# Kernel tuning notes

Hardware: AMD Instinct MI355X
Metric: run time of the kernel (lower is better)

Reference implementation:

```python
import jax, jax.numpy as jnp
import numpy as np

LOG2PI = float(np.log(2.0 * np.pi))

# Each Gaussian g is exp(-0.5*(a_g.x + b_g.y + c_g)^2)/sqrt(2*pi), with x the H current
# hidden variables and y the H next hidden variables. The original module applies a
# precompiled sequence of Givens-rotation 'gaussian products' (sequence_phase_1/2) that
# (phase 1) zero the x-coefficients of all but one pivot Gaussian per variable and
# integrate the pivots out, then (phase 2) rotate the leftover Gaussians so only H of
# them depend on y; leftover pure-bias Gaussians contribute norm_log_gaussian(bias).
# A sequence of Givens rotations is an orthogonal transform of the rows [a|b|c], so the
# whole procedure equals (up to per-row signs, which leave every Gaussian invariant):
#   QR on A -> integrate H pivots: LC1 = -sum_j log|R1_jj|
#   project B,c onto A's orthogonal complement, QR on PB -> kept rows (R2, Q2^T Pc)
#   residual bias energy -> LC2 = -0.5*((K-H)*log(2pi) + ||(P - Q2 Q2^T) c||^2)


def setup_inputs() -> dict:
    B, P, H, K, D = 2048, 4, 16, 48, 4
    key = jax.random.key(0)
    ks = jax.random.split(key, 8)
    f32 = jnp.float32
    return {
        "input_i": jax.random.normal(ks[0], (B, P, D), dtype=f32),
        "Prev_coefs": jax.random.normal(ks[1], (H, B, P, H), dtype=f32),
        "Prev_biases": jax.random.normal(ks[2], (H, B, P), dtype=f32),
        "LP": jnp.zeros((B, P), dtype=f32),
        "Log_factors": jax.random.normal(ks[3], (B, P), dtype=f32),
        "obs_var_coefs": jax.random.normal(ks[4], (K, B, P, D), dtype=f32),
        "hidden_var_coefs": jax.random.normal(ks[5], (K, B, P, H), dtype=f32),
        "next_hidden_var_coefs": jax.random.normal(ks[6], (K, B, P, H), dtype=f32),
        "rec_biases": jax.random.normal(ks[7], (K, B, P), dtype=f32),
    }


def reference(input_i, Prev_coefs, Prev_biases, LP, Log_factors,
              obs_var_coefs, hidden_var_coefs, next_hidden_var_coefs, rec_biases):
    H = Prev_coefs.shape[0]
    K = rec_biases.shape[0]
    # observation contribution to the recurrent Gaussians' biases: [K,B,P]
    cur_b = rec_biases + jnp.sum(obs_var_coefs * input_i[None], axis=-1)
    # stack all G = H + K Gaussians: coefs on current hidden vars (A), next hidden
    # vars (Bm) and biases (c). Previous-step Gaussians have zero next-var coefs.
    A = jnp.concatenate([Prev_coefs, hidden_var_coefs], axis=0)            # [G,B,P,H]
    Bm = jnp.concatenate([jnp.zeros_like(Prev_coefs), next_hidden_var_coefs], 0)
    c = jnp.concatenate([Prev_biases, cur_b], axis=0)                      # [G,B,P]
    A = jnp.moveaxis(A, 0, 2)   # [B,P,G,H]
    Bm = jnp.moveaxis(Bm, 0, 2)  # [B,P,G,H]
    c = jnp.moveaxis(c, 0, 2)   # [B,P,G]

    # phase 1: orthogonal elimination of the current-hidden-variable coefficients,
    # then integrate the H pivot Gaussians out.
    Q1, R1 = jnp.linalg.qr(A)                                              # Q1 [B,P,G,H]
    diag1 = jnp.abs(jnp.diagonal(R1, axis1=-2, axis2=-1))
    LC = -jnp.sum(jnp.log(diag1), axis=-1)                                 # [B,P]
    # project next-var coefs and biases onto the orthogonal complement of span(A)
    PB = Bm - Q1 @ (jnp.swapaxes(Q1, -1, -2) @ Bm)                         # [B,P,G,H]
    Pc = c - jnp.einsum('bpgh,bph->bpg', Q1, jnp.einsum('bpgh,bpg->bph', Q1, c))

    # phase 2: reduce the remaining K Gaussians to H kept ones.
    Q2, R2 = jnp.linalg.qr(PB)                                             # R2 [B,P,H,H]
    nb = jnp.einsum('bpgh,bpg->bph', Q2, Pc)                               # kept biases
    resid = jnp.maximum(jnp.sum(Pc * Pc, -1) - jnp.sum(nb * nb, -1), 0.0)
    # leftover (K - H) pure-bias Gaussians: sum of norm_log_gaussian(bias)
    LC = LC - 0.5 * ((K - H) * LOG2PI + resid)

    LP_new = LP + LC + Log_factors
    Next_coefs = jnp.moveaxis(R2, 2, 0)    # [H,B,P,H]
    Next_biases = jnp.moveaxis(nb, -1, 0)  # [H,B,P]
    return (Next_coefs, Next_biases, LP_new)
```

## Files before the change

kernel.cpp:

```cpp
#include <hip/hip_runtime.h>

#define LOG2PI 1.8378770664093453

__device__ __forceinline__ float rl32(float v, int l) {
  return __int_as_float(__builtin_amdgcn_readlane(__float_as_int(v), l));
}

__global__ __launch_bounds__(128, 6) void cint_kernel(
    const float* __restrict__ input_i,
    const float* __restrict__ Prev_coefs,
    const float* __restrict__ Prev_biases,
    const float* __restrict__ LPin,
    const float* __restrict__ Log_factors,
    const float* __restrict__ obs_var,
    const float* __restrict__ hid_var,
    const float* __restrict__ nxt_var,
    const float* __restrict__ rec_biases,
    float* __restrict__ out,
    int NBP)
{
  __shared__ float X[64*36];
  __shared__ float S[16*36];
  __shared__ float M2[2];

  const int tid  = threadIdx.x;
  const int w    = tid >> 6;
  const int lane = tid & 63;
  const int bid  = blockIdx.x;
  const int inst = (bid & 7) * (NBP >> 3) + (bid >> 3);

  float* PB = X;
  float* G  = S;

  const size_t NB_OFFv = (size_t)NBP * 256;
  const size_t LP_OFFv = NB_OFFv + (size_t)NBP * 16;

  const float lp_lf = LPin[inst] + Log_factors[inst];

  {
    const int g = lane;
    const size_t rowidx = (g < 16) ? ((size_t)g * NBP + inst)
                                   : ((size_t)(g - 16) * NBP + inst);
    if (w == 0) {
      const float* aptr = (g < 16) ? (Prev_coefs + rowidx * 16)
                                   : (hid_var    + rowidx * 16);
      *(float4*)&X[g*36 +  0] = *(const float4*)(aptr + 0);
      *(float4*)&X[g*36 +  4] = *(const float4*)(aptr + 4);
      *(float4*)&X[g*36 +  8] = *(const float4*)(aptr + 8);
      *(float4*)&X[g*36 + 12] = *(const float4*)(aptr + 12);
    } else {
      float4 z4 = make_float4(0.f, 0.f, 0.f, 0.f);
      float4 b0 = z4, b1 = z4, b2 = z4, b3 = z4;
      float cv;
      if (g < 16) {
        cv = Prev_biases[rowidx];
      } else {
        const float* bptr = nxt_var + rowidx * 16;
        b0 = *(const float4*)(bptr + 0);
        b1 = *(const float4*)(bptr + 4);
        b2 = *(const float4*)(bptr + 8);
        b3 = *(const float4*)(bptr + 12);
        float4 ob = *(const float4*)(obs_var + rowidx * 4);
        float4 iv = *(const float4*)(input_i + (size_t)inst * 4);
        cv = rec_biases[rowidx] + ob.x*iv.x + ob.y*iv.y + ob.z*iv.z + ob.w*iv.w;
      }
      *(float4*)&X[g*36 + 16] = b0;
      *(float4*)&X[g*36 + 20] = b1;
      *(float4*)&X[g*36 + 24] = b2;
      *(float4*)&X[g*36 + 28] = b3;
      X[g*36 + 32] = cv;
    }
  }
  __syncthreads();

  {
    const int i  = tid & 15;
    const int st = tid >> 4;
    float ac0=0, ac1=0, ac2=0, ac3=0, ac4=0;
    #pragma unroll 8
    for (int g = 0; g < 64; ++g) {
      const float* xr = &X[g*36];
      float  xi = xr[i];
      float4 cv = *(const float4*)(xr + 4*st);
      ac0 = fmaf(xi, cv.x, ac0);
      ac1 = fmaf(xi, cv.y, ac1);
      ac2 = fmaf(xi, cv.z, ac2);
      ac3 = fmaf(xi, cv.w, ac3);
      if (st == 0) ac4 = fmaf(xi, xr[32], ac4);
    }
    float* srow = &S[i*36 + 4*st];
    srow[0]=ac0; srow[1]=ac1; srow[2]=ac2; srow[3]=ac3;
    if (st == 0) S[i*36 + 32] = ac4;
  }
  __syncthreads();

  if (w == 0) {
    float Lr[16];
    {
      const int ir = lane & 15;
      double prodd = 1.0;
      #pragma unroll
      for (int j = 0; j < 16; ++j) {
        float s = S[ir*36 + j];
        #pragma unroll
        for (int m = 0; m < j; ++m) s = fmaf(-Lr[m], rl32(Lr[m], j), s);
        float sj = rl32(s, j);
        sj = fmaxf(sj, 1e-30f);
        float Ljj = sqrtf(sj);
        float iv  = 1.0f / Ljj;
        prodd *= (double)sj;
        Lr[j] = (ir == j) ? Ljj : s * iv;
        if (lane == j) S[j*36 + 33] = iv;
      }
      if (lane == 0) M2[1] = (float)(-0.5 * log(prodd));
    }
    {
      const int rc = (lane < 17) ? lane : 16;
      float x[16];
      #pragma unroll
      for (int j = 0; j < 16; ++j) {
        float t = S[j*36 + 16 + rc];
        #pragma unroll
        for (int m = 0; m < j; ++m) t = fmaf(-rl32(Lr[m], j), x[m], t);
        x[j] = t * S[j*36 + 33];
      }
      #pragma unroll
      for (int j = 15; j >= 0; --j) {
        float t = x[j];
        #pragma unroll
        for (int m = j + 1; m < 16; ++m) t = fmaf(-rl32(Lr[j], m), x[m], t);
        x[j] = t * S[j*36 + 33];
      }
      if (lane < 17) {
        #pragma unroll
        for (int m = 0; m < 16; ++m) S[m*36 + 16 + lane] = x[m];
      }
    }
  }
  __syncthreads();

  {
    const int g = lane;
    const float* xr = &X[g*36];
    float4 a0 = *(const float4*)(xr + 0);
    float4 a1 = *(const float4*)(xr + 4);
    float4 a2 = *(const float4*)(xr + 8);
    float4 a3 = *(const float4*)(xr + 12);
    float ad[16] = { a0.x,a0.y,a0.z,a0.w, a1.x,a1.y,a1.z,a1.w,
                     a2.x,a2.y,a2.z,a2.w, a3.x,a3.y,a3.z,a3.w };
    float4 e0, e1; float pc = 0.0f;
    if (w == 0) {
      e0 = *(const float4*)(xr + 16);
      e1 = *(const float4*)(xr + 20);
    } else {
      e0 = *(const float4*)(xr + 24);
      e1 = *(const float4*)(xr + 28);
      pc = xr[32];
    }
    float pb[8] = { e0.x,e0.y,e0.z,e0.w, e1.x,e1.y,e1.z,e1.w };
    __syncthreads();
    const int coff = 16 + 8*w;
    #pragma unroll
    for (int m = 0; m < 16; ++m) {
      float am = ad[m];
      float4 w0v = *(const float4*)(&S[m*36 + coff]);
      float4 w1v = *(const float4*)(&S[m*36 + coff + 4]);
      pb[0] = fmaf(-am, w0v.x, pb[0]); pb[1] = fmaf(-am, w0v.y, pb[1]);
      pb[2] = fmaf(-am, w0v.z, pb[2]); pb[3] = fmaf(-am, w0v.w, pb[3]);
      pb[4] = fmaf(-am, w1v.x, pb[4]); pb[5] = fmaf(-am, w1v.y, pb[5]);
      pb[6] = fmaf(-am, w1v.z, pb[6]); pb[7] = fmaf(-am, w1v.w, pb[7]);
      if (w == 1) pc = fmaf(-am, S[m*36 + 32], pc);
    }
    if (w == 1) {
      float q = pc * pc;
      #pragma unroll
      for (int msk = 1; msk < 64; msk <<= 1) q += __shfl_xor(q, msk, 64);
      if (lane == 0) M2[0] = q;
    }
    float4 o0 = { pb[0], pb[1], pb[2], pb[3] };
    float4 o1 = { pb[4], pb[5], pb[6], pb[7] };
    *(float4*)&PB[g*20 + 8*w + 0] = o0;
    *(float4*)&PB[g*20 + 8*w + 4] = o1;
    if (w == 1) PB[g*20 + 16] = pc;
  }
  __syncthreads();

  {
    const int k1 = tid & 15;
    const int q  = tid >> 4;
    float ac0=0, ac1=0, ac4=0;
    #pragma unroll 8
    for (int g = 0; g < 64; ++g) {
      const float* pr = &PB[g*20];
      float  xr = pr[k1];
      float2 cv = *(const float2*)(pr + 2*q);
      ac0 = fmaf(xr, cv.x, ac0);
      ac1 = fmaf(xr, cv.y, ac1);
      if (q == 0) ac4 = fmaf(xr, pr[16], ac4);
    }
    G[k1*18 + 2*q]     = ac0;
    G[k1*18 + 2*q + 1] = ac1;
    if (q == 0) G[k1*18 + 16] = ac4;
  }
  __syncthreads();

  if (w == 0) {
    const int k  = lane;
    const int kc = (k < 17) ? k : 16;
    float Tr[16];
    float Gh[16];
    #pragma unroll
    for (int r = 0; r < 16; ++r) Tr[r] = PB[r*20 + kc];
    #pragma unroll
    for (int j = 0; j < 16; ++j) Gh[j] = G[j*18 + kc];
    float nbacc = 0.0f;
    #pragma unroll
    for (int j = 0; j < 16; ++j) {
      float alf  = rl32(Tr[j], j);
      float nrm2 = rl32(Gh[j], j);
      float nrm  = sqrtf(fmaxf(nrm2, 1e-30f));
      float aa   = fabsf(alf);
      float tau  = 1.0f + aa / nrm;
      float inv  = copysignf(1.0f / (aa + nrm), alf);
      float beta = -copysignf(nrm, alf);
      float Tj   = Tr[j];
      float wv   = Tj + (Gh[j] - alf * Tj) * inv;
      float Rv   = Tj - tau * wv;
      if (k < 16) {
        float ov = (k < j) ? 0.0f : ((k == j) ? beta : Rv);
        out[((size_t)j * NBP + inst) * 16 + k] = ov;
      } else if (k == 16) {
        out[NB_OFFv + (size_t)j * NBP + inst] = Rv;
        nbacc = fmaf(Rv, Rv, nbacc);
      }
      float twi = tau * wv * inv;
      #pragma unroll
      for (int r = j + 1; r < 16; ++r) {
        float vr = rl32(Tr[r], j);
        Tr[r] = fmaf(-twi, vr, Tr[r]);
      }
      #pragma unroll
      for (int l = j + 1; l < 16; ++l) {
        float Rl = rl32(Rv, l);
        Gh[l] = fmaf(-Rl, Rv, Gh[l]);
      }
    }
    if (k == 16) {
      double resid = fmax((double)M2[0] - (double)nbacc, 0.0);
      double LC = (double)M2[1] - 0.5 * (32.0 * LOG2PI + resid);
      out[LP_OFFv + (size_t)inst] = lp_lf + (float)LC;
    }
  }
}

extern "C" void kernel_launch(void* const* d_in, const int* in_sizes, int n_in,
                              void* d_out, int out_size, void* d_ws, size_t ws_size,
                              hipStream_t stream) {
  (void)n_in; (void)out_size; (void)d_ws; (void)ws_size;
  const int NBP = in_sizes[3];
  cint_kernel<<<NBP, 128, 0, stream>>>(
      (const float*)d_in[0], (const float*)d_in[1], (const float*)d_in[2],
      (const float*)d_in[3], (const float*)d_in[4], (const float*)d_in[5],
      (const float*)d_in[6], (const float*)d_in[7], (const float*)d_in[8],
      (float*)d_out, NBP);
}
```

Baseline: 186.4 us.

## Compute full Gram matrix once and derive projected Gram via Schur complement

Instead of forming the projected matrix PB explicitly over all 64 rows and then computing its Gram matrix, the kernel computes the full 33x33 symmetric Gram of [A|B|c] once (lower triangle split across threads) and obtains the projected Gram and the top rows of PB through triangular solves with the Cholesky factor (Schur complement). This drops one 64-row pass and the back-substitution, shares a single LDS buffer, and raises the occupancy hint to 7. In exchange it relies on the Gram/Schur formulation being numerically adequate, and it adds slot-mapping overhead and extra LDS transposes.

```diff
diff --git a/kernel.cpp b/kernel.cpp
--- a/kernel.cpp
+++ b/kernel.cpp
@@ -6,7 +6,30 @@
   return __int_as_float(__builtin_amdgcn_readlane(__float_as_int(v), l));
 }
 
-__global__ __launch_bounds__(128, 6) void cint_kernel(
+#define OFF_M33   0
+#define OFF_STAB  1188
+#define OFF_T     1188
+#define OFF_Y     1508
+#define OFF_Z     1828
+#define OFF_G     2148
+#define OFF_CTOP  2454
+#define OFF_ATOPT 2470
+#define OFF_M2    2790
+#define LDSZ      2792
+
+__device__ __forceinline__ void slot_to_rq(int s, int& r, int& q) {
+  if      (s < 4)   { r = s;               q = 0;    }
+  else if (s < 12)  { int i=s-4;   r=4 +i/2; q=i-(i/2)*2; }
+  else if (s < 24)  { int i=s-12;  r=8 +i/3; q=i-(i/3)*3; }
+  else if (s < 40)  { int i=s-24;  r=12+(i>>2); q=i&3; }
+  else if (s < 60)  { int i=s-40;  r=16+i/5; q=i-(i/5)*5; }
+  else if (s < 84)  { int i=s-60;  r=20+i/6; q=i-(i/6)*6; }
+  else if (s < 112) { int i=s-84;  r=24+i/7; q=i-(i/7)*7; }
+  else if (s < 144) { int i=s-112; r=28+(i>>3); q=i&7; }
+  else              { r = 32; q = s-144; }
+}
+
+__global__ __launch_bounds__(128, 7) void cint_kernel(
     const float* __restrict__ input_i,
     const float* __restrict__ Prev_coefs,
     const float* __restrict__ Prev_biases,
@@ -19,18 +42,13 @@
     float* __restrict__ out,
     int NBP)
 {
-  __shared__ float X[64*36];
-  __shared__ float S[16*36];
-  __shared__ float M2[2];
+  __shared__ float lds[LDSZ];
 
   const int tid  = threadIdx.x;
   const int w    = tid >> 6;
   const int lane = tid & 63;
   const int bid  = blockIdx.x;
   const int inst = (bid & 7) * (NBP >> 3) + (bid >> 3);
-
-  float* PB = X;
-  float* G  = S;
 
   const size_t NB_OFFv = (size_t)NBP * 256;
   const size_t LP_OFFv = NB_OFFv + (size_t)NBP * 16;
@@ -44,16 +62,31 @@
     if (w == 0) {
       const float* aptr = (g < 16) ? (Prev_coefs + rowidx * 16)
                                    : (hid_var    + rowidx * 16);
-      *(float4*)&X[g*36 +  0] = *(const float4*)(aptr + 0);
-      *(float4*)&X[g*36 +  4] = *(const float4*)(aptr + 4);
-      *(float4*)&X[g*36 +  8] = *(const float4*)(aptr + 8);
-      *(float4*)&X[g*36 + 12] = *(const float4*)(aptr + 12);
+      float4 a0 = *(const float4*)(aptr + 0);
+      float4 a1 = *(const float4*)(aptr + 4);
+      float4 a2 = *(const float4*)(aptr + 8);
+      float4 a3 = *(const float4*)(aptr + 12);
+      *(float4*)&lds[g*36 +  0] = a0;
+      *(float4*)&lds[g*36 +  4] = a1;
+      *(float4*)&lds[g*36 +  8] = a2;
+      *(float4*)&lds[g*36 + 12] = a3;
+      if (g < 16) {
+        lds[OFF_ATOPT +  0*20+g]=a0.x; lds[OFF_ATOPT +  1*20+g]=a0.y;
+        lds[OFF_ATOPT +  2*20+g]=a0.z; lds[OFF_ATOPT +  3*20+g]=a0.w;
+        lds[OFF_ATOPT +  4*20+g]=a1.x; lds[OFF_ATOPT +  5*20+g]=a1.y;
+        lds[OFF_ATOPT +  6*20+g]=a1.z; lds[OFF_ATOPT +  7*20+g]=a1.w;
+        lds[OFF_ATOPT +  8*20+g]=a2.x; lds[OFF_ATOPT +  9*20+g]=a2.y;
+        lds[OFF_ATOPT + 10*20+g]=a2.z; lds[OFF_ATOPT + 11*20+g]=a2.w;
+        lds[OFF_ATOPT + 12*20+g]=a3.x; lds[OFF_ATOPT + 13*20+g]=a3.y;
+        lds[OFF_ATOPT + 14*20+g]=a3.z; lds[OFF_ATOPT + 15*20+g]=a3.w;
+      }
     } else {
       float4 z4 = make_float4(0.f, 0.f, 0.f, 0.f);
       float4 b0 = z4, b1 = z4, b2 = z4, b3 = z4;
       float cv;
       if (g < 16) {
         cv = Prev_biases[rowidx];
+        lds[OFF_CTOP + g] = cv;
       } else {
         const float* bptr = nxt_var + rowidx * 16;
         b0 = *(const float4*)(bptr + 0);
@@ -64,33 +97,65 @@
         float4 iv = *(const float4*)(input_i + (size_t)inst * 4);
         cv = rec_biases[rowidx] + ob.x*iv.x + ob.y*iv.y + ob.z*iv.z + ob.w*iv.w;
       }
-      *(float4*)&X[g*36 + 16] = b0;
-      *(float4*)&X[g*36 + 20] = b1;
-      *(float4*)&X[g*36 + 24] = b2;
-      *(float4*)&X[g*36 + 28] = b3;
-      X[g*36 + 32] = cv;
-    }
-  }
-  __syncthreads();
-
-  {
-    const int i  = tid & 15;
-    const int st = tid >> 4;
-    float ac0=0, ac1=0, ac2=0, ac3=0, ac4=0;
+      *(float4*)&lds[g*36 + 16] = b0;
+      *(float4*)&lds[g*36 + 20] = b1;
+      *(float4*)&lds[g*36 + 24] = b2;
+      *(float4*)&lds[g*36 + 28] = b3;
+      lds[g*36 + 32] = cv;
+      lds[g*36 + 33] = 0.f; lds[g*36 + 34] = 0.f; lds[g*36 + 35] = 0.f;
+    }
+  }
+  __syncthreads();
+
+  int r0, q0; slot_to_rq(tid, r0, q0);
+  float a00=0,a01=0,a02=0,a03=0;
+  {
     #pragma unroll 8
     for (int g = 0; g < 64; ++g) {
-      const float* xr = &X[g*36];
-      float  xi = xr[i];
-      float4 cv = *(const float4*)(xr + 4*st);
-      ac0 = fmaf(xi, cv.x, ac0);
-      ac1 = fmaf(xi, cv.y, ac1);
-      ac2 = fmaf(xi, cv.z, ac2);
-      ac3 = fmaf(xi, cv.w, ac3);
-      if (st == 0) ac4 = fmaf(xi, xr[32], ac4);
-    }
-    float* srow = &S[i*36 + 4*st];
-    srow[0]=ac0; srow[1]=ac1; srow[2]=ac2; srow[3]=ac3;
-    if (st == 0) S[i*36 + 32] = ac4;
+      const float* xr = &lds[g*36];
+      float  xi = xr[r0];
+      float4 cv = *(const float4*)(xr + 4*q0);
+      a00=fmaf(xi,cv.x,a00); a01=fmaf(xi,cv.y,a01);
+      a02=fmaf(xi,cv.z,a02); a03=fmaf(xi,cv.w,a03);
+    }
+  }
+  const bool has2 = (tid >= 103);
+  int r1=0, q1=0;
+  float a10=0,a11=0,a12=0,a13=0;
+  if (has2) {
+    slot_to_rq(tid + 25, r1, q1);
+    #pragma unroll 8
+    for (int g = 0; g < 64; ++g) {
+      const float* xr = &lds[g*36];
+      float  xi = xr[r1];
+      float4 cv = *(const float4*)(xr + 4*q1);
+      a10=fmaf(xi,cv.x,a10); a11=fmaf(xi,cv.y,a11);
+      a12=fmaf(xi,cv.z,a12); a13=fmaf(xi,cv.w,a13);
+    }
+  }
+  __syncthreads();
+
+  {
+    float4 v0 = make_float4(a00,a01,a02,a03);
+    *(float4*)&lds[OFF_M33 + r0*36 + 4*q0] = v0;
+    if (r0 >= 16 && q0 < 4) {
+      const int k = r0 - 16;
+      lds[OFF_STAB + (4*q0+0)*20 + k] = a00;
+      lds[OFF_STAB + (4*q0+1)*20 + k] = a01;
+      lds[OFF_STAB + (4*q0+2)*20 + k] = a02;
+      lds[OFF_STAB + (4*q0+3)*20 + k] = a03;
+    }
+    if (has2) {
+      float4 v1 = make_float4(a10,a11,a12,a13);
+      *(float4*)&lds[OFF_M33 + r1*36 + 4*q1] = v1;
+      if (r1 >= 16 && q1 < 4) {
+        const int k = r1 - 16;
+        lds[OFF_STAB + (4*q1+0)*20 + k] = a10;
+        lds[OFF_STAB + (4*q1+1)*20 + k] = a11;
+        lds[OFF_STAB + (4*q1+2)*20 + k] = a12;
+        lds[OFF_STAB + (4*q1+3)*20 + k] = a13;
+      }
+    }
   }
   __syncthreads();
 
@@ -101,106 +166,64 @@
       double prodd = 1.0;
       #pragma unroll
       for (int j = 0; j < 16; ++j) {
-        float s = S[ir*36 + j];
+        float s = lds[OFF_M33 + ((ir >= j) ? (ir*36 + j) : (j*36 + ir))];
         #pragma unroll
         for (int m = 0; m < j; ++m) s = fmaf(-Lr[m], rl32(Lr[m], j), s);
-        float sj = rl32(s, j);
-        sj = fmaxf(sj, 1e-30f);
+        float sj = fmaxf(rl32(s, j), 1e-30f);
         float Ljj = sqrtf(sj);
         float iv  = 1.0f / Ljj;
         prodd *= (double)sj;
         Lr[j] = (ir == j) ? Ljj : s * iv;
-        if (lane == j) S[j*36 + 33] = iv;
-      }
-      if (lane == 0) M2[1] = (float)(-0.5 * log(prodd));
+        if (lane == j) lds[OFF_M33 + j*36 + 33] = iv;
+      }
+      if (lane == 0) lds[OFF_M2 + 1] = (float)(-0.5 * log(prodd));
     }
     {
-      const int rc = (lane < 17) ? lane : 16;
+      const bool isY = (lane < 17);
+      const int  ci  = isY ? lane : ((lane - 17 < 15) ? lane - 17 : 15);
+      const float* ip = isY ? &lds[OFF_STAB + ci] : &lds[OFF_ATOPT + ci];
       float x[16];
       #pragma unroll
       for (int j = 0; j < 16; ++j) {
-        float t = S[j*36 + 16 + rc];
+        float t = ip[j*20];
         #pragma unroll
         for (int m = 0; m < j; ++m) t = fmaf(-rl32(Lr[m], j), x[m], t);
-        x[j] = t * S[j*36 + 33];
-      }
-      #pragma unroll
-      for (int j = 15; j >= 0; --j) {
-        float t = x[j];
-        #pragma unroll
-        for (int m = j + 1; m < 16; ++m) t = fmaf(-rl32(Lr[j], m), x[m], t);
-        x[j] = t * S[j*36 + 33];
-      }
-      if (lane < 17) {
-        #pragma unroll
-        for (int m = 0; m < 16; ++m) S[m*36 + 16 + lane] = x[m];
-      }
-    }
-  }
-  __syncthreads();
-
-  {
-    const int g = lane;
-    const float* xr = &X[g*36];
-    float4 a0 = *(const float4*)(xr + 0);
-    float4 a1 = *(const float4*)(xr + 4);
-    float4 a2 = *(const float4*)(xr + 8);
-    float4 a3 = *(const float4*)(xr + 12);
-    float ad[16] = { a0.x,a0.y,a0.z,a0.w, a1.x,a1.y,a1.z,a1.w,
-                     a2.x,a2.y,a2.z,a2.w, a3.x,a3.y,a3.z,a3.w };
-    float4 e0, e1; float pc = 0.0f;
-    if (w == 0) {
-      e0 = *(const float4*)(xr + 16);
-      e1 = *(const float4*)(xr + 20);
-    } else {
-      e0 = *(const float4*)(xr + 24);
-      e1 = *(const float4*)(xr + 28);
-      pc = xr[32];
-    }
-    float pb[8] = { e0.x,e0.y,e0.z,e0.w, e1.x,e1.y,e1.z,e1.w };
-    __syncthreads();
-    const int coff = 16 + 8*w;
-    #pragma unroll
-    for (int m = 0; m < 16; ++m) {
-      float am = ad[m];
-      float4 w0v = *(const float4*)(&S[m*36 + coff]);
-      float4 w1v = *(const float4*)(&S[m*36 + coff + 4]);
-      pb[0] = fmaf(-am, w0v.x, pb[0]); pb[1] = fmaf(-am, w0v.y, pb[1]);
-      pb[2] = fmaf(-am, w0v.z, pb[2]); pb[3] = fmaf(-am, w0v.w, pb[3]);
-      pb[4] = fmaf(-am, w1v.x, pb[4]); pb[5] = fmaf(-am, w1v.y, pb[5]);
-      pb[6] = fmaf(-am, w1v.z, pb[6]); pb[7] = fmaf(-am, w1v.w, pb[7]);
-      if (w == 1) pc = fmaf(-am, S[m*36 + 32], pc);
-    }
-    if (w == 1) {
-      float q = pc * pc;
-      #pragma unroll
-      for (int msk = 1; msk < 64; msk <<= 1) q += __shfl_xor(q, msk, 64);
-      if (lane == 0) M2[0] = q;
-    }
-    float4 o0 = { pb[0], pb[1], pb[2], pb[3] };
-    float4 o1 = { pb[4], pb[5], pb[6], pb[7] };
-    *(float4*)&PB[g*20 + 8*w + 0] = o0;
-    *(float4*)&PB[g*20 + 8*w + 4] = o1;
-    if (w == 1) PB[g*20 + 16] = pc;
-  }
-  __syncthreads();
-
-  {
-    const int k1 = tid & 15;
-    const int q  = tid >> 4;
-    float ac0=0, ac1=0, ac4=0;
-    #pragma unroll 8
-    for (int g = 0; g < 64; ++g) {
-      const float* pr = &PB[g*20];
-      float  xr = pr[k1];
-      float2 cv = *(const float2*)(pr + 2*q);
-      ac0 = fmaf(xr, cv.x, ac0);
-      ac1 = fmaf(xr, cv.y, ac1);
-      if (q == 0) ac4 = fmaf(xr, pr[16], ac4);
-    }
-    G[k1*18 + 2*q]     = ac0;
-    G[k1*18 + 2*q + 1] = ac1;
-    if (q == 0) G[k1*18 + 16] = ac4;
+        x[j] = t * lds[OFF_M33 + j*36 + 33];
+      }
+      if (lane < 33) {
+        float* op = isY ? &lds[OFF_Y + ci] : &lds[OFF_Z + ci];
+        #pragma unroll
+        for (int m = 0; m < 16; ++m) op[m*20] = x[m];
+      }
+    }
+  }
+  __syncthreads();
+
+  for (int s = tid; s < 153; s += 128) {
+    float fs = 8.f * (float)s + 1.f;
+    int k = (int)((sqrtf(fs) - 1.f) * 0.5f);
+    int l = s - ((k * (k + 1)) >> 1);
+    float acc = lds[OFF_M33 + (16 + k)*36 + 16 + l];
+    #pragma unroll
+    for (int m = 0; m < 16; ++m)
+      acc = fmaf(-lds[OFF_Y + m*20 + k], lds[OFF_Y + m*20 + l], acc);
+    lds[OFF_G + k*18 + l] = acc;
+    lds[OFF_G + l*18 + k] = acc;
+  }
+  {
+    #pragma unroll
+    for (int p = 0; p < 4; ++p) {
+      int s = p * 128 + tid;
+      int r  = s >> 5;
+      int kk = s & 31;
+      if (kk < 17) {
+        float acc = (kk == 16) ? lds[OFF_CTOP + r] : 0.f;
+        #pragma unroll
+        for (int m = 0; m < 16; ++m)
+          acc = fmaf(-lds[OFF_Z + m*20 + r], lds[OFF_Y + m*20 + kk], acc);
+        lds[OFF_T + r*20 + kk] = acc;
+      }
+    }
   }
   __syncthreads();
 
@@ -210,9 +233,9 @@
     float Tr[16];
     float Gh[16];
     #pragma unroll
-    for (int r = 0; r < 16; ++r) Tr[r] = PB[r*20 + kc];
-    #pragma unroll
-    for (int j = 0; j < 16; ++j) Gh[j] = G[j*18 + kc];
+    for (int r = 0; r < 16; ++r) Tr[r] = lds[OFF_T + r*20 + kc];
+    #pragma unroll
+    for (int j = 0; j < 16; ++j) Gh[j] = lds[OFF_G + j*18 + kc];
     float nbacc = 0.0f;
     #pragma unroll
     for (int j = 0; j < 16; ++j) {
@@ -246,8 +269,8 @@
       }
     }
     if (k == 16) {
-      double resid = fmax((double)M2[0] - (double)nbacc, 0.0);
-      double LC = (double)M2[1] - 0.5 * (32.0 * LOG2PI + resid);
+      double resid = fmax((double)lds[OFF_G + 16*18 + 16] - (double)nbacc, 0.0);
+      double LC = (double)lds[OFF_M2 + 1] - 0.5 * (32.0 * LOG2PI + resid);
       out[LP_OFFv + (size_t)inst] = lp_lf + (float)LC;
     }
   }
```

After: 177.0 us. 1.05x faster.
